# Optimization experiments

Measured on AMD Instinct MI355X. Metric: run time of the kernel, lower is better.

The kernel has to match this reference:

```python
import jax, jax.numpy as jnp
import numpy as np

B, S, E, DQ, DV = 8, 2048, 1024, 128, 128


def setup_inputs() -> dict:
    k0 = jax.random.key(0)
    ks = jax.random.split(k0, 10)
    scale_in = 1.0 / np.sqrt(E)
    return {
        "pad_mask": jax.random.uniform(ks[0], (B, S)) < 0.1,  # True = padded key position
        "query": jax.random.normal(ks[1], (B, S, E), jnp.float32),
        "key": jax.random.normal(ks[2], (B, S, E), jnp.float32),
        "value": jax.random.normal(ks[3], (B, S, E), jnp.float32),
        "Wq": jax.random.uniform(ks[4], (E, DQ), jnp.float32, -scale_in, scale_in),
        "bq": jnp.zeros((DQ,), jnp.float32),
        "Wk": jax.random.uniform(ks[5], (E, DQ), jnp.float32, -scale_in, scale_in),
        "bk": jnp.zeros((DQ,), jnp.float32),
        "Wv": jax.random.uniform(ks[6], (E, DV), jnp.float32, -scale_in, scale_in),
        "bv": jnp.zeros((DV,), jnp.float32),
    }


def reference(pad_mask, query, key, value, Wq, bq, Wk, bk, Wv, bv):
    # Linear projections (torch Linear: x @ W^T + b; weights stored pre-transposed here)
    q = query @ Wq + bq  # [B,S,DQ]
    k = key @ Wk + bk    # [B,S,DQ]
    v = value @ Wv + bv  # [B,S,DV]

    scores = jnp.einsum("bqd,bkd->bqk", q, k)  # [B,S,S]
    # Causal mask applied BEFORE scaling (as in source); -inf/scale is still -inf
    seq = scores.shape[1]
    causal = jnp.triu(jnp.ones((seq, seq), bool), k=1)
    scores = jnp.where(causal[None], -jnp.inf, scores)
    scores = scores / jnp.asarray(q.shape[-1] ** 0.5, scores.dtype)
    # Padding mask: mask key positions with -1e9 (broadcast over query dim)
    scores = jnp.where(pad_mask[:, None, :], jnp.asarray(-1e9, scores.dtype), scores)

    attn = jax.nn.softmax(scores, axis=-1)
    return jnp.einsum("bqk,bkd->bqd", attn, v)  # [B,S,DV]
```

## Files before the change

kernel.cpp:

```cpp
#include <hip/hip_runtime.h>
#include <hip/hip_bf16.h>

#define SEQ 2048
#define EMB 1024
#define DH  128
#define QSCALE 0.08838834764831845f

typedef __attribute__((ext_vector_type(4))) float f32x4;
typedef __attribute__((ext_vector_type(8))) short bf16x8;
typedef __attribute__((ext_vector_type(4))) short bf16x4;

__device__ __forceinline__ short f2bf(float f) {
  unsigned u = __builtin_bit_cast(unsigned, f);
  u += 0x7fffu + ((u >> 16) & 1u);
  return (short)(u >> 16);
}

__device__ __forceinline__ float bf2f(short s) {
  unsigned u = ((unsigned)(unsigned short)s) << 16;
  return __builtin_bit_cast(float, u);
}

__device__ __forceinline__ f32x4 mfma16(bf16x8 a, bf16x8 b, f32x4 c) {
  return __builtin_amdgcn_mfma_f32_16x16x32_bf16(a, b, c, 0, 0, 0);
}

__device__ __forceinline__ void gl_lds16(void* lds_base, const void* gsrc) {
  __builtin_amdgcn_global_load_lds(
      (const __attribute__((address_space(1))) void*)gsrc,
      (__attribute__((address_space(3))) void*)lds_base, 16, 0, 0);
}

__global__ void prep_weights(const float* __restrict__ Wq, const float* __restrict__ Wk,
                             const float* __restrict__ Wv, short* __restrict__ wt) {
  int gid = blockIdx.x * 256 + threadIdx.x;
  int lane = gid & 63, c = lane & 15, g = (lane >> 4) & 3;
  int nb = (gid >> 6) & 7;
  int kk = (gid >> 9) & 31;
  int p = gid >> 14;
  const float* W = (p == 0) ? Wq : ((p == 1) ? Wk : Wv);
  bf16x8 v;
#pragma unroll
  for (int j = 0; j < 8; ++j)
    v[j] = f2bf(W[(kk * 32 + g * 8 + j) * DH + nb * 16 + c]);
  *(bf16x8*)(&wt[(size_t)gid * 8]) = v;
}

__global__ __launch_bounds__(256, 3) void proj_gemm(
    const float* __restrict__ Xq, const float* __restrict__ Xk, const float* __restrict__ Xv,
    const short* __restrict__ wt,
    const float* __restrict__ bq, const float* __restrict__ bk, const float* __restrict__ bv,
    short* __restrict__ qp, short* __restrict__ kp, short* __restrict__ vt) {
  __shared__ char wbuf[3][8192];

  const int tid = threadIdx.x;
  const int w = tid >> 6, lane = tid & 63;
  const int g = lane >> 4, c = lane & 15;
  const int bid = blockIdx.x;
  const int p = bid >> 8, mb = bid & 255;
  const int row0 = (mb << 6) + (w << 4);
  const float* X    = (p == 0) ? Xq : ((p == 1) ? Xk : Xv);
  const float* bias = (p == 0) ? bq : ((p == 1) ? bk : bv);
  const char* Ap = (const char*)X + (size_t)(row0 + c) * 4096 + (g << 5);
  const char* WT = (const char*)wt + (size_t)p * 262144;

  f32x4 acc[8];
#pragma unroll
  for (int nb = 0; nb < 8; ++nb) acc[nb] = (f32x4){0.f, 0.f, 0.f, 0.f};

  f32x4 aA0, aA1, aB0, aB1;

  auto loadA = [&](f32x4& a0, f32x4& a1, int t) {
    a0 = *(const f32x4*)(Ap + t * 128);
    a1 = *(const f32x4*)(Ap + t * 128 + 16);
  };

  auto stageW = [&](int buf, int t) {
#pragma unroll
    for (int i = 0; i < 2; ++i) {
      int ch = w + i * 4;
      gl_lds16(wbuf[buf] + ch * 1024,
               WT + (size_t)t * 8192 + ch * 1024 + lane * 16);
    }
  };

  auto computeT = [&](const f32x4& a0, const f32x4& a1, int buf) {
    bf16x8 a;
#pragma unroll
    for (int j = 0; j < 4; ++j) { a[j] = f2bf(a0[j]); a[4 + j] = f2bf(a1[j]); }
#pragma unroll
    for (int nb = 0; nb < 8; ++nb) {
      bf16x8 wfr = *(const bf16x8*)(wbuf[buf] + nb * 1024 + lane * 16);
      acc[nb] = mfma16(a, wfr, acc[nb]);
    }
  };

  loadA(aA0, aA1, 0);
  stageW(0, 0);
  __builtin_amdgcn_sched_barrier(0);

#pragma unroll 1
  for (int t = 0; t < 32; t += 2) {
    loadA(aB0, aB1, t + 1);
    stageW((t + 1) % 3, t + 1);
    __builtin_amdgcn_sched_barrier(0);
    asm volatile("s_waitcnt vmcnt(4)" ::: "memory");
    __builtin_amdgcn_sched_barrier(0);
    __builtin_amdgcn_s_barrier();
    computeT(aA0, aA1, t % 3);
    __builtin_amdgcn_sched_barrier(0);

    if (t + 2 < 32) {
      loadA(aA0, aA1, t + 2);
      stageW((t + 2) % 3, t + 2);
      __builtin_amdgcn_sched_barrier(0);
      asm volatile("s_waitcnt vmcnt(4)" ::: "memory");
    } else {
      asm volatile("s_waitcnt vmcnt(0)" ::: "memory");
    }
    __builtin_amdgcn_sched_barrier(0);
    __builtin_amdgcn_s_barrier();
    computeT(aB0, aB1, (t + 1) % 3);
    __builtin_amdgcn_sched_barrier(0);
  }

  float bvals[8];
#pragma unroll
  for (int nb = 0; nb < 8; ++nb) bvals[nb] = bias[nb * 16 + c];

  if (p < 2) {
    short* outp = (p == 0) ? qp : kp;
    float sc = (p == 0) ? QSCALE : 1.0f;
#pragma unroll
    for (int r = 0; r < 4; ++r) {
      int token = row0 + g * 4 + r;
#pragma unroll
      for (int nb = 0; nb < 8; ++nb)
        outp[token * 128 + nb * 16 + c] = f2bf((acc[nb][r] + bvals[nb]) * sc);
    }
  } else {
    int tok0 = row0 + g * 4;
    int b_ = tok0 >> 11, s_ = tok0 & 2047;
#pragma unroll
    for (int nb = 0; nb < 8; ++nb) {
      int col = nb * 16 + c;
      bf16x4 v4;
#pragma unroll
      for (int r = 0; r < 4; ++r) v4[r] = f2bf(acc[nb][r] + bvals[nb]);
      *(bf16x4*)(&vt[((size_t)(b_ * 128 + col)) * 2048 + s_]) = v4;
    }
  }
}

__global__ __launch_bounds__(256) void avgv2_kernel(
    const short* __restrict__ vt, const int* __restrict__ pad,
    const float* __restrict__ bvv, float* __restrict__ avgv) {
  int b = blockIdx.x >> 3, dg = blockIdx.x & 7;
  int t = threadIdx.x, doff = t >> 4, sl = t & 15;
  int d = dg * 16 + doff;
  const short* vrow = vt + ((size_t)(b * 128 + d)) * 2048 + sl * 128;
  const int* prow = pad + (b << 11) + sl * 128;
  float sum = 0.f;
  int cnt = 0;
  for (int i = 0; i < 16; ++i) {
    bf16x8 v8 = *(const bf16x8*)(vrow + i * 8);
#pragma unroll
    for (int j = 0; j < 8; ++j) {
      int pd = prow[i * 8 + j];
      cnt += (pd != 0);
      if (pd) sum += bf2f(v8[j]);
    }
  }
#pragma unroll
  for (int xm = 1; xm < 16; xm <<= 1) {
    sum += __shfl_xor(sum, xm, 64);
    cnt += __shfl_xor(cnt, xm, 64);
  }
  if (sl == 0) avgv[(b << 7) + d] = (cnt > 0) ? (sum / (float)cnt) : 0.f;
  (void)bvv;
}

__device__ __forceinline__ void stage_kv(short* kb, short* vb,
                                         const char* kb_base, const char* vb_base,
                                         int kt, int w, int lane) {
#pragma unroll
  for (int ch = w; ch < 16; ch += 4) {
    int phys = ch * 1024 + lane * 16;
    int lg = phys ^ (((phys >> 8) & 7) << 4);
    gl_lds16((char*)kb + ch * 1024,
             kb_base + (size_t)(kt * 64 + (lg >> 8)) * 256 + (lg & 255));
  }
#pragma unroll
  for (int ch = w; ch < 16; ch += 4) {
    int phys = ch * 1024 + lane * 16;
    int lg = phys ^ (((phys >> 7) & 7) << 4);
    gl_lds16((char*)vb + ch * 1024,
             vb_base + (size_t)(lg >> 7) * 4096 + kt * 128 + (lg & 127));
  }
}

template <bool CAUSAL>
__device__ __forceinline__ void attn_tile(
    const short* __restrict__ k_lds, const short* __restrict__ v_lds, short* __restrict__ p_w,
    const bf16x8 (&qf)[4], f32x4 (&acc_o)[8], float (&m_r)[4], float (&l_r)[4],
    const int* __restrict__ padp, int kt, int qrow_g, int g, int c) {
  f32x4 sc[4];
#pragma unroll
  for (int nb = 0; nb < 4; ++nb) sc[nb] = (f32x4){0.f, 0.f, 0.f, 0.f};
#pragma unroll
  for (int ks = 0; ks < 4; ++ks) {
    bf16x8 kf[4];
#pragma unroll
    for (int nb = 0; nb < 4; ++nb) {
      int n = (nb << 4) + c;
      int off = (n << 8) + (ks << 6) + (g << 4);
      kf[nb] = *(const bf16x8*)((const char*)k_lds + (off ^ ((n & 7) << 4)));
    }
#pragma unroll
    for (int nb = 0; nb < 4; ++nb) sc[nb] = mfma16(qf[ks], kf[nb], sc[nb]);
  }

  int padv[4];
#pragma unroll
  for (int nb = 0; nb < 4; ++nb) padv[nb] = padp[kt + (nb << 4) + c];
  float sv[4][4];
#pragma unroll
  for (int nb = 0; nb < 4; ++nb) {
    bool pd = padv[nb] != 0;
    int key = kt + (nb << 4) + c;
#pragma unroll
    for (int r = 0; r < 4; ++r) {
      float s = sc[nb][r];
      if (CAUSAL && key > qrow_g + r) s = -1e30f;
      if (pd) s = -1e30f;
      sv[nb][r] = s;
    }
  }
  float tmax[4];
#pragma unroll
  for (int r = 0; r < 4; ++r)
    tmax[r] = fmaxf(fmaxf(sv[0][r], sv[1][r]), fmaxf(sv[2][r], sv[3][r]));
#pragma unroll
  for (int xm = 1; xm < 16; xm <<= 1)
#pragma unroll
    for (int r = 0; r < 4; ++r) tmax[r] = fmaxf(tmax[r], __shfl_xor(tmax[r], xm, 64));
  float al[4];
#pragma unroll
  for (int r = 0; r < 4; ++r) {
    float mn = fmaxf(m_r[r], tmax[r]);
    al[r] = __expf(m_r[r] - mn);
    m_r[r] = mn;
  }
  float ls[4] = {0.f, 0.f, 0.f, 0.f};
#pragma unroll
  for (int nb = 0; nb < 4; ++nb)
#pragma unroll
    for (int r = 0; r < 4; ++r) {
      float pp = __expf(sv[nb][r] - m_r[r]);
      sv[nb][r] = pp;
      ls[r] += pp;
    }
#pragma unroll
  for (int xm = 1; xm < 16; xm <<= 1)
#pragma unroll
    for (int r = 0; r < 4; ++r) ls[r] += __shfl_xor(ls[r], xm, 64);
#pragma unroll
  for (int r = 0; r < 4; ++r) l_r[r] = l_r[r] * al[r] + ls[r];
#pragma unroll
  for (int nb = 0; nb < 8; ++nb)
#pragma unroll
    for (int r = 0; r < 4; ++r) acc_o[nb][r] *= al[r];

#pragma unroll
  for (int nb = 0; nb < 4; ++nb)
#pragma unroll
    for (int r = 0; r < 4; ++r)
      p_w[(g * 4 + r) * 72 + (nb << 4) + c] = f2bf(sv[nb][r]);

#pragma unroll
  for (int ks = 0; ks < 2; ++ks) {
    bf16x8 pa = *(const bf16x8*)((const char*)p_w + c * 144 + ks * 64 + g * 16);
#pragma unroll
    for (int nb = 0; nb < 8; ++nb) {
      int n = (nb << 4) + c;
      int off = (n << 7) + (ks << 6) + (g << 4);
      bf16x8 vf = *(const bf16x8*)((const char*)v_lds + (off ^ ((n & 7) << 4)));
      acc_o[nb] = mfma16(pa, vf, acc_o[nb]);
    }
  }
}

__global__ __launch_bounds__(256) void flash_attn(
    const short* __restrict__ qp, const short* __restrict__ kp, const short* __restrict__ vt,
    const int* __restrict__ pad, float* __restrict__ partO, float* __restrict__ partML) {
  __shared__ short k_lds[2][64 * 128];
  __shared__ short v_lds[2][128 * 64];
  __shared__ short p_lds[4][16 * 72];
  const int tid = threadIdx.x, w = tid >> 6, lane = tid & 63;
  const int g = lane >> 4, c = lane & 15;
  const int j = blockIdx.x;
  int b, qi, half;
  if (j < 256) { b = j >> 5; qi = j & 31; half = 0; }
  else { int u = j - 256; b = u >> 5; qi = 31 - (u & 31); half = 1; }
  const int T = qi + 1;
  const int t0 = half ? (T >> 1) : 0;
  const int t1 = half ? T : (T >> 1);
  const int q0 = qi << 6;

  bf16x8 qf[4];
  {
    int token = (b << 11) + q0 + (w << 4) + c;
    const char* qrow = (const char*)qp + (size_t)token * 256;
#pragma unroll
    for (int s = 0; s < 4; ++s) qf[s] = *(const bf16x8*)(qrow + s * 64 + g * 16);
  }
  f32x4 acc_o[8];
#pragma unroll
  for (int i = 0; i < 8; ++i) acc_o[i] = (f32x4){0.f, 0.f, 0.f, 0.f};
  float m_r[4] = {-1e30f, -1e30f, -1e30f, -1e30f};
  float l_r[4] = {0.f, 0.f, 0.f, 0.f};

  const char* kb_base = (const char*)kp + (size_t)(b << 11) * 256;
  const char* vb_base = (const char*)vt + (size_t)b * 524288;
  const int* padp = pad + (b << 11);
  const int qrow_g = q0 + (w << 4) + (g << 2);

  if (t1 > t0) {
    stage_kv(k_lds[0], v_lds[0], kb_base, vb_base, t0, w, lane);
    __syncthreads();
    int cur = 0;
    for (int t = t0; t < t1; ++t) {
      if (t + 1 < t1)
        stage_kv(k_lds[cur ^ 1], v_lds[cur ^ 1], kb_base, vb_base, t + 1, w, lane);
      if (half && t == T - 1)
        attn_tile<true>(k_lds[cur], v_lds[cur], p_lds[w], qf, acc_o, m_r, l_r,
                        padp, t << 6, qrow_g, g, c);
      else
        attn_tile<false>(k_lds[cur], v_lds[cur], p_lds[w], qf, acc_o, m_r, l_r,
                         padp, t << 6, qrow_g, g, c);
      __syncthreads();
      cur ^= 1;
    }
  }

  float* pO = partO + (size_t)j * (64 * 128);
  float* pML = partML + (size_t)j * 128;
#pragma unroll
  for (int nb = 0; nb < 8; ++nb)
#pragma unroll
    for (int r = 0; r < 4; ++r)
      pO[(w * 16 + g * 4 + r) * 128 + (nb << 4) + c] = acc_o[nb][r];
  if (c == 0)
#pragma unroll
    for (int r = 0; r < 4; ++r) {
      pML[(w * 16 + g * 4 + r) * 2] = m_r[r];
      pML[(w * 16 + g * 4 + r) * 2 + 1] = l_r[r];
    }
}

__global__ __launch_bounds__(256) void combine_kernel(
    const float* __restrict__ partO, const float* __restrict__ partML,
    const float* __restrict__ avgv, float* __restrict__ out) {
  int gid = blockIdx.x * 256 + threadIdx.x;
  int row = gid >> 5;
  int d4 = gid & 31;
  int b = row >> 11, s = row & 2047;
  int qt = s >> 6, lr = s & 63;
  int wid1 = (b << 5) + qt;
  int wid2 = 256 + (b << 5) + (31 - qt);
  float m1 = partML[wid1 * 128 + lr * 2], l1 = partML[wid1 * 128 + lr * 2 + 1];
  float m2 = partML[wid2 * 128 + lr * 2], l2 = partML[wid2 * 128 + lr * 2 + 1];
  float m = fmaxf(m1, m2);
  f32x4 o;
  if (m < -1e8f) {
    o = *(const f32x4*)(avgv + (b << 7) + (d4 << 2));
  } else {
    float f1 = __expf(m1 - m), f2 = __expf(m2 - m);
    float inv = 1.0f / (l1 * f1 + l2 * f2);
    f32x4 o1 = *(const f32x4*)(partO + ((size_t)wid1 * 64 + lr) * 128 + (d4 << 2));
    f32x4 o2 = *(const f32x4*)(partO + ((size_t)wid2 * 64 + lr) * 128 + (d4 << 2));
#pragma unroll
    for (int k = 0; k < 4; ++k) o[k] = (o1[k] * f1 + o2[k] * f2) * inv;
  }
  *(f32x4*)(out + (size_t)row * 128 + (d4 << 2)) = o;
}

extern "C" void kernel_launch(void* const* d_in, const int* in_sizes, int n_in,
                              void* d_out, int out_size, void* d_ws, size_t ws_size,
                              hipStream_t stream) {
  const int*   pad   = (const int*)d_in[0];
  const float* query = (const float*)d_in[1];
  const float* key   = (const float*)d_in[2];
  const float* value = (const float*)d_in[3];
  const float* Wq    = (const float*)d_in[4];
  const float* bq    = (const float*)d_in[5];
  const float* Wk    = (const float*)d_in[6];
  const float* bk    = (const float*)d_in[7];
  const float* Wv    = (const float*)d_in[8];
  const float* bv    = (const float*)d_in[9];
  char* ws = (char*)d_ws;
  short* wt    = (short*)ws;
  short* qp    = (short*)(ws + 786432);
  short* kp    = (short*)(ws + 4980736);
  short* vt    = (short*)(ws + 9175040);
  float* partO = (float*)(ws + 13369344);
  float* partML= (float*)(ws + 30146560);
  float* avgv  = (float*)(ws + 30408704);
  float* out   = (float*)d_out;

  prep_weights<<<dim3(192), dim3(256), 0, stream>>>(Wq, Wk, Wv, wt);
  proj_gemm<<<dim3(768), dim3(256), 0, stream>>>(query, key, value, wt, bq, bk, bv, qp, kp, vt);
  avgv2_kernel<<<dim3(64), dim3(256), 0, stream>>>(vt, pad, bv, avgv);
  flash_attn<<<dim3(512), dim3(256), 0, stream>>>(qp, kp, vt, pad, partO, partML);
  combine_kernel<<<dim3(2048), dim3(256), 0, stream>>>(partO, partML, avgv, out);
}
```

Measured before the change: 98.54 us.

## Restructure projection GEMM: 16-row tiles staged whole in LDS, weights streamed to registers

The projection GEMM now gives each block a 16-row tile of fp32 activations, loading the whole tile (64KB) into LDS with an XOR swizzle to avoid bank conflicts. Each wave computes two 16-column output blocks and streams its weight fragments straight from global memory into registers, triple-buffered. This removes the per-step block barriers and LDS weight staging, and launches 4x more blocks. In exchange each weight fragment is re-read from global/L2 by every block, and the large LDS footprint cuts occupancy to about two blocks per CU.

```diff
diff --git a/kernel.cpp b/kernel.cpp
--- a/kernel.cpp
+++ b/kernel.cpp
@@ -46,109 +46,104 @@
   *(bf16x8*)(&wt[(size_t)gid * 8]) = v;
 }
 
-__global__ __launch_bounds__(256, 3) void proj_gemm(
+__global__ __launch_bounds__(256, 2) void proj_gemm(
     const float* __restrict__ Xq, const float* __restrict__ Xk, const float* __restrict__ Xv,
     const short* __restrict__ wt,
     const float* __restrict__ bq, const float* __restrict__ bk, const float* __restrict__ bv,
     short* __restrict__ qp, short* __restrict__ kp, short* __restrict__ vt) {
-  __shared__ char wbuf[3][8192];
+  __shared__ char a_lds[65536];
 
   const int tid = threadIdx.x;
   const int w = tid >> 6, lane = tid & 63;
   const int g = lane >> 4, c = lane & 15;
   const int bid = blockIdx.x;
-  const int p = bid >> 8, mb = bid & 255;
-  const int row0 = (mb << 6) + (w << 4);
+  const int p = bid >> 10, tile = bid & 1023;
+  const int row0 = tile << 4;
   const float* X    = (p == 0) ? Xq : ((p == 1) ? Xk : Xv);
   const float* bias = (p == 0) ? bq : ((p == 1) ? bk : bv);
-  const char* Ap = (const char*)X + (size_t)(row0 + c) * 4096 + (g << 5);
+  const char* Xt = (const char*)X + (size_t)tile * 65536;
   const char* WT = (const char*)wt + (size_t)p * 262144;
-
-  f32x4 acc[8];
-#pragma unroll
-  for (int nb = 0; nb < 8; ++nb) acc[nb] = (f32x4){0.f, 0.f, 0.f, 0.f};
-
-  f32x4 aA0, aA1, aB0, aB1;
-
-  auto loadA = [&](f32x4& a0, f32x4& a1, int t) {
-    a0 = *(const f32x4*)(Ap + t * 128);
-    a1 = *(const f32x4*)(Ap + t * 128 + 16);
+  const char* Wp = WT + (size_t)(w * 2) * 1024;
+
+  f32x4 acc[2];
+  acc[0] = (f32x4){0.f, 0.f, 0.f, 0.f};
+  acc[1] = (f32x4){0.f, 0.f, 0.f, 0.f};
+
+  bf16x8 wrA[2], wrB[2], wrC[2];
+
+  auto loadW = [&](bf16x8* dst, int kk) {
+#pragma unroll
+    for (int i = 0; i < 2; ++i)
+      dst[i] = *(const bf16x8*)(Wp + (size_t)kk * 8192 + i * 1024 + (lane << 4));
   };
 
-  auto stageW = [&](int buf, int t) {
-#pragma unroll
-    for (int i = 0; i < 2; ++i) {
-      int ch = w + i * 4;
-      gl_lds16(wbuf[buf] + ch * 1024,
-               WT + (size_t)t * 8192 + ch * 1024 + lane * 16);
-    }
+  auto computeK = [&](const bf16x8* wf, int kk) {
+    int ad = ((kk << 7) + (g << 5)) ^ ((c & 15) << 4);
+    const char* arow = a_lds + (c << 12);
+    f32x4 lo = *(const f32x4*)(arow + ad);
+    f32x4 hi = *(const f32x4*)(arow + (ad ^ 16));
+    bf16x8 a;
+#pragma unroll
+    for (int j = 0; j < 4; ++j) { a[j] = f2bf(lo[j]); a[4 + j] = f2bf(hi[j]); }
+    acc[0] = mfma16(a, wf[0], acc[0]);
+    acc[1] = mfma16(a, wf[1], acc[1]);
   };
 
-  auto computeT = [&](const f32x4& a0, const f32x4& a1, int buf) {
-    bf16x8 a;
-#pragma unroll
-    for (int j = 0; j < 4; ++j) { a[j] = f2bf(a0[j]); a[4 + j] = f2bf(a1[j]); }
-#pragma unroll
-    for (int nb = 0; nb < 8; ++nb) {
-      bf16x8 wfr = *(const bf16x8*)(wbuf[buf] + nb * 1024 + lane * 16);
-      acc[nb] = mfma16(a, wfr, acc[nb]);
-    }
-  };
-
-  loadA(aA0, aA1, 0);
-  stageW(0, 0);
+#pragma unroll
+  for (int i = 0; i < 16; ++i) {
+    int id = (w << 4) | i;
+    int row = id >> 2, q = id & 3;
+    gl_lds16(a_lds + (row << 12) + (q << 10),
+             Xt + (row << 12) + (q << 10) + ((lane << 4) ^ ((row & 15) << 4)));
+  }
+  loadW(wrA, 0);
+  loadW(wrB, 1);
+  loadW(wrC, 2);
   __builtin_amdgcn_sched_barrier(0);
-
-#pragma unroll 1
-  for (int t = 0; t < 32; t += 2) {
-    loadA(aB0, aB1, t + 1);
-    stageW((t + 1) % 3, t + 1);
+  asm volatile("s_waitcnt vmcnt(4)" ::: "memory");
+  __builtin_amdgcn_sched_barrier(0);
+  __builtin_amdgcn_s_barrier();
+
+#pragma unroll
+  for (int kk = 0; kk < 32; ++kk) {
+    if (kk > 0) {
+      if (kk <= 29)      asm volatile("s_waitcnt vmcnt(4)" ::: "memory");
+      else if (kk == 30) asm volatile("s_waitcnt vmcnt(2)" ::: "memory");
+      else               asm volatile("s_waitcnt vmcnt(0)" ::: "memory");
+      __builtin_amdgcn_sched_barrier(0);
+    }
+    const bf16x8* wf = (kk % 3 == 0) ? wrA : ((kk % 3 == 1) ? wrB : wrC);
+    computeK(wf, kk);
     __builtin_amdgcn_sched_barrier(0);
-    asm volatile("s_waitcnt vmcnt(4)" ::: "memory");
-    __builtin_amdgcn_sched_barrier(0);
-    __builtin_amdgcn_s_barrier();
-    computeT(aA0, aA1, t % 3);
-    __builtin_amdgcn_sched_barrier(0);
-
-    if (t + 2 < 32) {
-      loadA(aA0, aA1, t + 2);
-      stageW((t + 2) % 3, t + 2);
+    if (kk + 3 < 32) {
+      bf16x8* dst = (kk % 3 == 0) ? wrA : ((kk % 3 == 1) ? wrB : wrC);
+      loadW(dst, kk + 3);
       __builtin_amdgcn_sched_barrier(0);
-      asm volatile("s_waitcnt vmcnt(4)" ::: "memory");
-    } else {
-      asm volatile("s_waitcnt vmcnt(0)" ::: "memory");
-    }
-    __builtin_amdgcn_sched_barrier(0);
-    __builtin_amdgcn_s_barrier();
-    computeT(aB0, aB1, (t + 1) % 3);
-    __builtin_amdgcn_sched_barrier(0);
-  }
-
-  float bvals[8];
-#pragma unroll
-  for (int nb = 0; nb < 8; ++nb) bvals[nb] = bias[nb * 16 + c];
-
+    }
+  }
+
+  int n0 = (w << 1) + 0, n1 = (w << 1) + 1;
+  float bv0 = bias[n0 * 16 + c], bv1 = bias[n1 * 16 + c];
   if (p < 2) {
     short* outp = (p == 0) ? qp : kp;
     float sc = (p == 0) ? QSCALE : 1.0f;
 #pragma unroll
     for (int r = 0; r < 4; ++r) {
       int token = row0 + g * 4 + r;
-#pragma unroll
-      for (int nb = 0; nb < 8; ++nb)
-        outp[token * 128 + nb * 16 + c] = f2bf((acc[nb][r] + bvals[nb]) * sc);
+      outp[token * 128 + n0 * 16 + c] = f2bf((acc[0][r] + bv0) * sc);
+      outp[token * 128 + n1 * 16 + c] = f2bf((acc[1][r] + bv1) * sc);
     }
   } else {
     int tok0 = row0 + g * 4;
     int b_ = tok0 >> 11, s_ = tok0 & 2047;
-#pragma unroll
-    for (int nb = 0; nb < 8; ++nb) {
-      int col = nb * 16 + c;
-      bf16x4 v4;
-#pragma unroll
-      for (int r = 0; r < 4; ++r) v4[r] = f2bf(acc[nb][r] + bvals[nb]);
-      *(bf16x4*)(&vt[((size_t)(b_ * 128 + col)) * 2048 + s_]) = v4;
-    }
+    bf16x4 v0, v1;
+#pragma unroll
+    for (int r = 0; r < 4; ++r) {
+      v0[r] = f2bf(acc[0][r] + bv0);
+      v1[r] = f2bf(acc[1][r] + bv1);
+    }
+    *(bf16x4*)(&vt[((size_t)(b_ * 128 + n0 * 16 + c)) * 2048 + s_]) = v0;
+    *(bf16x4*)(&vt[((size_t)(b_ * 128 + n1 * 16 + c)) * 2048 + s_]) = v1;
   }
 }
 
@@ -409,7 +404,7 @@
   float* out   = (float*)d_out;
 
   prep_weights<<<dim3(192), dim3(256), 0, stream>>>(Wq, Wk, Wv, wt);
-  proj_gemm<<<dim3(768), dim3(256), 0, stream>>>(query, key, value, wt, bq, bk, bv, qp, kp, vt);
+  proj_gemm<<<dim3(3072), dim3(256), 0, stream>>>(query, key, value, wt, bq, bk, bv, qp, kp, vt);
   avgv2_kernel<<<dim3(64), dim3(256), 0, stream>>>(vt, pad, bv, avgv);
   flash_attn<<<dim3(512), dim3(256), 0, stream>>>(qp, kp, vt, pad, partO, partML);
   combine_kernel<<<dim3(2048), dim3(256), 0, stream>>>(partO, partML, avgv, out);
```

After: 120.1 us. 1.22x slower.
